# Optimization experiments

Hardware: AMD Instinct MI355X
Metric: run time of the kernel (lower is better)

Reference implementation:

```python
import jax, jax.numpy as jnp
import numpy as np

TOP_K = 2  # cfg.num_experts_per_tok
INIT_STD = 0.02


def setup_inputs() -> dict:
    key = jax.random.key(0)
    ks = jax.random.split(key, 6)
    B, S, D, F, E = 4, 2048, 1024, 4096, 8
    return {
        "residual": jax.random.normal(ks[0], (B, S, D), dtype=jnp.float32),
        "W_router": jax.random.normal(ks[1], (E, D), dtype=jnp.float32) * INIT_STD,
        "W_in": jax.random.normal(ks[2], (E, D, F), dtype=jnp.float32) * INIT_STD,
        "b_in": jnp.zeros((E, F), dtype=jnp.float32),
        "W_out": jax.random.normal(ks[3], (E, F, D), dtype=jnp.float32) * INIT_STD,
        "b_out": jnp.zeros((E, D), dtype=jnp.float32),
    }


def reference(residual, W_router, W_in, b_in, W_out, b_out):
    B, S, D = residual.shape
    E = W_router.shape[0]
    x = residual.reshape(-1, D)                      # [T, D], T = B*S

    # Router: softmax over experts, pick top-k, renormalize selected weights.
    logits = jnp.einsum('td,ed->te', x, W_router)    # [T, E]
    probs = jax.nn.softmax(logits, axis=-1)
    top_w, top_i = jax.lax.top_k(probs, TOP_K)       # [T, K]
    top_w = top_w / jnp.sum(top_w, axis=-1, keepdims=True)

    # Dense combine weights [T, E]; zero for non-selected experts.
    combine = jnp.sum(jax.nn.one_hot(top_i, E, dtype=x.dtype) * top_w[..., None], axis=1)

    # Weighted sum of expert MLP outputs (GELU experts, exact erf as in torch).
    y = jnp.zeros_like(x)
    for e in range(E):  # small fixed expert count
        h = jax.nn.gelu(x @ W_in[e] + b_in[e], approximate=False)   # [T, F]
        y = y + combine[:, e:e + 1] * (h @ W_out[e] + b_out[e])     # [T, D]
    return y.reshape(B, S, D)
```

## Files before the change

kernel.cpp:

```cpp
#include <hip/hip_runtime.h>
#include <hip/hip_bf16.h>
#include <math.h>

#define T_TOK 8192
#define DMODEL 1024
#define FFN 4096
#define NEXP 8
#define NSLOT (T_TOK * 2)
#define MAXT 136

typedef _Float16 f16;
typedef _Float16 half8 __attribute__((ext_vector_type(8)));
typedef _Float16 half4 __attribute__((ext_vector_type(4)));
typedef float f32x4 __attribute__((ext_vector_type(4)));
typedef unsigned int u32;

__device__ __forceinline__ void gll16(const void* g, void* l) {
  __builtin_amdgcn_global_load_lds(
      (const __attribute__((address_space(1))) u32*)g,
      (__attribute__((address_space(3))) u32*)l, 16, 0, 0);
}

__device__ __forceinline__ float gelu_fast(float v) {
  float x = fabsf(v) * 0.70710678118654752f;
  float t = 1.0f / (1.0f + 0.3275911f * x);
  float poly = ((((1.061405429f * t - 1.453152027f) * t + 1.421413741f) * t -
                 0.284496736f) * t + 0.254829592f) * t;
  float erf_ = 1.0f - poly * __expf(-x * x);
  erf_ = copysignf(erf_, v);
  return 0.5f * v * (1.0f + erf_);
}

__device__ __forceinline__ float gelu_exact(float v) {
  return 0.5f * v * (1.0f + erff(v * 0.70710678118654752f));
}

__device__ __forceinline__ void transq_tile(const float* __restrict__ ip,
                                            f16* __restrict__ op, int R, int C,
                                            int r0, int c0, char* smemraw) {
  float* tile = (float*)smemraw;
  int tid = threadIdx.x;
  int q = tid & 15;
  int rr = tid >> 4;
#pragma unroll
  for (int p = 0; p < 8; p++) {
    int row = rr + p * 16;
    float4 v = *(const float4*)(ip + (size_t)(r0 + row) * C + c0 + q * 4);
    int qs = (q + (row >> 3)) & 15;
    *(float4*)(tile + row * 64 + qs * 4) = v;
  }
  __syncthreads();
#pragma unroll
  for (int p = 0; p < 4; p++) {
    int idx = tid + p * 256;
    int c = idx >> 4;
    int b = idx & 15;
    half8 h;
#pragma unroll
    for (int i = 0; i < 8; i++) {
      int row = b * 8 + i;
      int qs = (((c >> 2) + b) & 15);
      h[i] = (f16)tile[row * 64 + qs * 4 + (c & 3)];
    }
    *(half8*)(op + (size_t)(c0 + c) * R + r0 + b * 8) = h;
  }
}

__global__ __launch_bounds__(256) void prepA_k(
    const float* __restrict__ x, const float* __restrict__ Wr,
    const float* __restrict__ Wi,
    int* __restrict__ sel_e, float* __restrict__ sel_w,
    f16* __restrict__ xh, f16* __restrict__ WiT) {
  __shared__ __align__(16) char smem[32768];
  if (blockIdx.x < 4096) {
    int e = blockIdx.x >> 9;
    int idx = blockIdx.x & 511;
    int rt = idx >> 6, ct = idx & 63;
    transq_tile(Wi + (size_t)e * DMODEL * FFN, WiT + (size_t)e * DMODEL * FFN,
                DMODEL, FFN, rt * 128, ct * 64, smem);
  } else {
    int rb = blockIdx.x - 4096;
    int t = rb * 4 + (threadIdx.x >> 6);
    int lane = threadIdx.x & 63;
    const float* xp = x + (size_t)t * DMODEL;
    f16* xhp = xh + (size_t)t * DMODEL;
    float p[NEXP];
#pragma unroll
    for (int e = 0; e < NEXP; e++) p[e] = 0.f;
#pragma unroll
    for (int q = 0; q < 4; q++) {
      float4 xv = *(const float4*)(xp + q * 256 + lane * 4);
      half4 h;
      h[0] = (f16)xv.x; h[1] = (f16)xv.y; h[2] = (f16)xv.z; h[3] = (f16)xv.w;
      *(half4*)(xhp + q * 256 + lane * 4) = h;
#pragma unroll
      for (int e = 0; e < NEXP; e++) {
        float4 wv = *(const float4*)(Wr + e * DMODEL + q * 256 + lane * 4);
        p[e] += xv.x * wv.x + xv.y * wv.y + xv.z * wv.z + xv.w * wv.w;
      }
    }
#pragma unroll
    for (int off = 32; off; off >>= 1) {
#pragma unroll
      for (int e = 0; e < NEXP; e++) p[e] += __shfl_xor(p[e], off);
    }
    if (lane == 0) {
      float l0 = -1e30f, l1 = -1e30f;
      int e0 = 0, e1 = 1;
#pragma unroll
      for (int e = 0; e < NEXP; e++) {
        if (p[e] > l0) { l1 = l0; e1 = e0; l0 = p[e]; e0 = e; }
        else if (p[e] > l1) { l1 = p[e]; e1 = e; }
      }
      float r = expf(l1 - l0);
      float inv = 1.f / (1.f + r);
      sel_e[t * 2] = e0;     sel_w[t * 2] = inv;
      sel_e[t * 2 + 1] = e1; sel_w[t * 2 + 1] = r * inv;
    }
  }
}

__global__ __launch_bounds__(256) void count8_k(const int* __restrict__ sel_e,
                                                int* __restrict__ counts) {
  int e = blockIdx.x;
  int tid = threadIdx.x;
  int c = 0;
  for (int i = tid; i < NSLOT; i += 256) c += (sel_e[i] == e) ? 1 : 0;
#pragma unroll
  for (int off = 32; off; off >>= 1) c += __shfl_down(c, off);
  __shared__ int red[4];
  if ((tid & 63) == 0) red[tid >> 6] = c;
  __syncthreads();
  if (tid == 0) counts[e] = red[0] + red[1] + red[2] + red[3];
}

__global__ void sched_k(int* meta) {
  int* counts = meta;
  int* fill = meta + 64;
  int* offs = meta + 128;
  int* tE = meta + 256;
  int* tR0 = meta + 512;
  int* tRows = meta + 768;
  int off = 0, nt = 0;
  for (int e = 0; e < NEXP; e++) {
    offs[e] = off;
    fill[e] = 0;
    int c = counts[e];
    for (int t0 = 0; t0 < c; t0 += 128) {
      tE[nt] = e; tR0[nt] = off + t0; tRows[nt] = min(128, c - t0); nt++;
    }
    off += c;
  }
  offs[NEXP] = off;
  for (; nt < MAXT; nt++) tE[nt] = -1;
}

__global__ __launch_bounds__(256) void scatter_k(
    const int* __restrict__ sel_e, const float* __restrict__ sel_w,
    const int* __restrict__ offs, int* fill,
    int* __restrict__ row_tok, float* __restrict__ row_w) {
  int s = blockIdx.x * 256 + threadIdx.x;
  int e = sel_e[s];
  int pos = atomicAdd(&fill[e], 1);
  int r = offs[e] + pos;
  row_tok[r] = s >> 1;
  row_w[r] = sel_w[s];
}

__global__ __launch_bounds__(256, 3) void gemm1_k(
    const f16* __restrict__ Xh, const f16* __restrict__ Wt,
    const float* __restrict__ b_in, f16* __restrict__ H,
    const int* __restrict__ meta,
    const float* __restrict__ Wo, f16* __restrict__ WoT) {
  __shared__ __align__(16) char smem[33792];

  if (blockIdx.x < 4096) {
    int e = blockIdx.x >> 9;
    int idx = blockIdx.x & 511;
    int rt = idx >> 4, ct = idx & 15;
    transq_tile(Wo + (size_t)e * DMODEL * FFN, WoT + (size_t)e * DMODEL * FFN,
                FFN, DMODEL, rt * 128, ct * 64, smem);
    return;
  }
  int bid2 = blockIdx.x - 4096;
  int xcd = bid2 & 7, bidx = bid2 >> 3;
  int wg = xcd * ((MAXT * 32) >> 3) + bidx;
  int tm = wg >> 5;
  int n0 = (wg & 31) * 128;
  int e = (meta + 256)[tm];
  if (e < 0) return;
  int row0 = (meta + 512)[tm];
  int nrows = (meta + 768)[tm];
  const int* row_tok = meta + 1024 + 2 * NSLOT;

  int tid = threadIdx.x, lane = tid & 63, wid = tid >> 6;
  int wrow = wid >> 1, wcol = wid & 1;
  int l15 = lane & 15, l4 = lane >> 4;

  u32 aoffs[4], boffs[4];
#pragma unroll
  for (int p = 0; p < 4; p++) {
    int L = tid + p * 256;
    int row = L >> 3, ch = L & 7;
    int cs = ch ^ (row & 7);
    aoffs[p] = (u32)(row_tok[min(row0 + row, NSLOT - 1)] * (DMODEL * 2) + cs * 16);
    boffs[p] = (u32)((e * FFN + n0 + row) * (DMODEL * 2) + cs * 16);
  }
  const char* gA = (const char*)Xh;
  const char* gB = (const char*)Wt;

  f32x4 acc[4][4];
#pragma unroll
  for (int m = 0; m < 4; m++)
#pragma unroll
    for (int n = 0; n < 4; n++) acc[m][n] = (f32x4)0.f;

  const int NT = DMODEL / 64;
  for (int kt = 0; kt < NT; ++kt) {
#pragma unroll
    for (int p = 0; p < 4; p++) {
      gll16(gA + aoffs[p], smem + (tid + p * 256) * 16);
      gll16(gB + boffs[p], smem + 16384 + (tid + p * 256) * 16);
      aoffs[p] += 128; boffs[p] += 128;
    }
    __syncthreads();
#pragma unroll
    for (int s = 0; s < 2; s++) {
      int swz = ((s * 4 + l4) ^ (l15 & 7)) << 4;
      const char* pA = smem + (wrow * 64 + l15) * 128 + swz;
      const char* pB = smem + 16384 + (wcol * 64 + l15) * 128 + swz;
      half8 a[4], b[4];
#pragma unroll
      for (int i = 0; i < 4; i++) a[i] = *(const half8*)(pA + i * 2048);
#pragma unroll
      for (int j = 0; j < 4; j++) b[j] = *(const half8*)(pB + j * 2048);
#pragma unroll
      for (int i = 0; i < 4; i++)
#pragma unroll
        for (int j = 0; j < 4; j++)
          acc[i][j] = __builtin_amdgcn_mfma_f32_16x16x32_f16(a[i], b[j], acc[i][j], 0, 0, 0);
    }
    __syncthreads();
  }

  float bias[4];
#pragma unroll
  for (int n = 0; n < 4; n++) bias[n] = b_in[e * FFN + n0 + wcol * 64 + n * 16 + l15];
#pragma unroll
  for (int m = 0; m < 4; m++)
#pragma unroll
    for (int n = 0; n < 4; n++)
#pragma unroll
      for (int j = 0; j < 4; j++) {
        int row = wrow * 64 + m * 16 + l4 * 4 + j;
        int col = wcol * 64 + n * 16 + l15;
        *(f16*)(smem + row * 264 + col * 2) = (f16)gelu_fast(acc[m][n][j] + bias[n]);
      }
  __syncthreads();
#pragma unroll
  for (int p = 0; p < 8; ++p) {
    int idx = tid + p * 256;
    int row = idx >> 4, cc = idx & 15;
    if (row < nrows) {
      f32x4 v = *(const f32x4*)(smem + row * 264 + cc * 16);
      __builtin_nontemporal_store(
          v, (f32x4*)(H + (size_t)(row0 + row) * FFN + n0 + cc * 8));
    }
  }
}

__global__ __launch_bounds__(256, 3) void gemm2_k(
    const f16* __restrict__ H, const f16* __restrict__ Wt,
    const float* __restrict__ b_out, float* __restrict__ out,
    const int* __restrict__ meta) {
  int xcd = blockIdx.x & 7, bidx = blockIdx.x >> 3;
  int wg = xcd * (gridDim.x >> 3) + bidx;
  int tm = wg >> 4;
  int r4 = wg & 15;
  int n0 = (r4 & 7) * 128;
  int ks = r4 >> 3;
  int e = (meta + 256)[tm];
  if (e < 0) return;
  int row0 = (meta + 512)[tm];
  int nrows = (meta + 768)[tm];
  const int* row_tok = meta + 1024 + 2 * NSLOT;
  const float* row_w = (const float*)(meta + 1024 + 3 * NSLOT);

  __shared__ __align__(16) char smem[32768];

  int tid = threadIdx.x, lane = tid & 63, wid = tid >> 6;
  int wrow = wid >> 1, wcol = wid & 1;
  int l15 = lane & 15, l4 = lane >> 4;
  u32 k0b = (u32)(ks * (FFN / 2) * 2);

  u32 aoffs[4], boffs[4];
#pragma unroll
  for (int p = 0; p < 4; p++) {
    int L = tid + p * 256;
    int row = L >> 3, ch = L & 7;
    int cs = ch ^ (row & 7);
    aoffs[p] = (u32)((u32)min(row0 + row, NSLOT - 1) * (FFN * 2) + k0b + cs * 16);
    boffs[p] = (u32)((u32)(e * DMODEL + n0 + row) * (FFN * 2) + k0b + cs * 16);
  }
  const char* gA = (const char*)H;
  const char* gB = (const char*)Wt;

  f32x4 acc[4][4];
#pragma unroll
  for (int m = 0; m < 4; m++)
#pragma unroll
    for (int n = 0; n < 4; n++) acc[m][n] = (f32x4)0.f;

  const int NT = (FFN / 2) / 64;
  for (int kt = 0; kt < NT; ++kt) {
#pragma unroll
    for (int p = 0; p < 4; p++) {
      gll16(gA + aoffs[p], smem + (tid + p * 256) * 16);
      gll16(gB + boffs[p], smem + 16384 + (tid + p * 256) * 16);
      aoffs[p] += 128; boffs[p] += 128;
    }
    __syncthreads();
#pragma unroll
    for (int s = 0; s < 2; s++) {
      int swz = ((s * 4 + l4) ^ (l15 & 7)) << 4;
      const char* pA = smem + (wrow * 64 + l15) * 128 + swz;
      const char* pB = smem + 16384 + (wcol * 64 + l15) * 128 + swz;
      half8 a[4], b[4];
#pragma unroll
      for (int i = 0; i < 4; i++) a[i] = *(const half8*)(pA + i * 2048);
#pragma unroll
      for (int j = 0; j < 4; j++) b[j] = *(const half8*)(pB + j * 2048);
#pragma unroll
      for (int i = 0; i < 4; i++)
#pragma unroll
        for (int j = 0; j < 4; j++)
          acc[i][j] = __builtin_amdgcn_mfma_f32_16x16x32_f16(a[i], b[j], acc[i][j], 0, 0, 0);
    }
    __syncthreads();
  }

  float bias[4];
#pragma unroll
  for (int n = 0; n < 4; n++)
    bias[n] = (ks == 0) ? b_out[e * DMODEL + n0 + wcol * 64 + n * 16 + l15] : 0.f;
#pragma unroll
  for (int m = 0; m < 4; m++)
#pragma unroll
    for (int j = 0; j < 4; j++) {
      int r = wrow * 64 + m * 16 + l4 * 4 + j;
      if (r < nrows) {
        int rg = row0 + r;
        int tok = row_tok[rg];
        float w = row_w[rg];
#pragma unroll
        for (int n = 0; n < 4; n++)
          atomicAdd(out + (size_t)tok * DMODEL + n0 + wcol * 64 + n * 16 + l15,
                    w * (acc[m][n][j] + bias[n]));
      }
    }
}

__global__ __launch_bounds__(256) void naive_k(
    const float* __restrict__ x, const float* __restrict__ W_in,
    const float* __restrict__ b_in, const float* __restrict__ W_out,
    const float* __restrict__ b_out, const int* __restrict__ sel_e,
    const float* __restrict__ sel_w, float* __restrict__ out) {
  int s = blockIdx.x;
  int t = s >> 1;
  int e = sel_e[s];
  float w = sel_w[s];
  __shared__ float xs[DMODEL];
  __shared__ float hs[FFN];
  int tid = threadIdx.x;
  for (int d = tid; d < DMODEL; d += 256) xs[d] = x[(size_t)t * DMODEL + d];
  __syncthreads();
  for (int f = tid; f < FFN; f += 256) {
    float a = b_in[e * FFN + f];
    const float* wp = W_in + (size_t)e * DMODEL * FFN + f;
    for (int d = 0; d < DMODEL; d++) a += xs[d] * wp[(size_t)d * FFN];
    hs[f] = gelu_exact(a);
  }
  __syncthreads();
  for (int d = tid; d < DMODEL; d += 256) {
    float a = b_out[e * DMODEL + d];
    const float* wp = W_out + (size_t)e * FFN * DMODEL + d;
    for (int f = 0; f < FFN; f++) a += hs[f] * wp[(size_t)f * DMODEL];
    atomicAdd(&out[(size_t)t * DMODEL + d], w * a);
  }
}

__global__ __launch_bounds__(256) void router_k(
    const float* __restrict__ x, const float* __restrict__ Wr,
    int* __restrict__ sel_e, float* __restrict__ sel_w) {
  int t = blockIdx.x * 4 + (threadIdx.x >> 6);
  int lane = threadIdx.x & 63;
  const float* xp = x + (size_t)t * DMODEL;
  float p[NEXP];
#pragma unroll
  for (int e = 0; e < NEXP; e++) p[e] = 0.f;
#pragma unroll
  for (int i = 0; i < DMODEL / 64; i++) {
    float xv = xp[lane + i * 64];
#pragma unroll
    for (int e = 0; e < NEXP; e++) p[e] += xv * Wr[e * DMODEL + lane + i * 64];
  }
#pragma unroll
  for (int off = 32; off; off >>= 1) {
#pragma unroll
    for (int e = 0; e < NEXP; e++) p[e] += __shfl_xor(p[e], off);
  }
  if (lane == 0) {
    float l0 = -1e30f, l1 = -1e30f;
    int e0 = 0, e1 = 1;
#pragma unroll
    for (int e = 0; e < NEXP; e++) {
      if (p[e] > l0) { l1 = l0; e1 = e0; l0 = p[e]; e0 = e; }
      else if (p[e] > l1) { l1 = p[e]; e1 = e; }
    }
    float r = expf(l1 - l0);
    float inv = 1.f / (1.f + r);
    sel_e[t * 2] = e0;     sel_w[t * 2] = inv;
    sel_e[t * 2 + 1] = e1; sel_w[t * 2 + 1] = r * inv;
  }
}

extern "C" void kernel_launch(void* const* d_in, const int* in_sizes, int n_in,
                              void* d_out, int out_size, void* d_ws, size_t ws_size,
                              hipStream_t stream) {
  const float* residual = (const float*)d_in[0];
  const float* W_router = (const float*)d_in[1];
  const float* W_in = (const float*)d_in[2];
  const float* b_in = (const float*)d_in[3];
  const float* W_out = (const float*)d_in[4];
  const float* b_out = (const float*)d_in[5];
  float* out = (float*)d_out;

  char* ws = (char*)d_ws;
  int* meta = (int*)ws;
  size_t off = (size_t)1 << 20;
  f16* Xh = (f16*)(ws + off); off += (size_t)T_TOK * DMODEL * 2;
  f16* Wih = (f16*)(ws + off); off += (size_t)NEXP * DMODEL * FFN * 2;
  f16* Woh = (f16*)(ws + off); off += (size_t)NEXP * DMODEL * FFN * 2;
  f16* H = (f16*)(ws + off); off += (size_t)NSLOT * FFN * 2;
  off += 65536;
  bool fast = ws_size >= off;

  int* sel_e = meta + 1024;
  float* sel_w = (float*)(meta + 1024 + NSLOT);
  int* row_tok = meta + 1024 + 2 * NSLOT;
  float* row_w = (float*)(meta + 1024 + 3 * NSLOT);

  hipMemsetAsync(meta, 0, 4096, stream);
  hipMemsetAsync(d_out, 0, (size_t)out_size * sizeof(float), stream);

  if (fast) {
    prepA_k<<<4096 + T_TOK / 4, 256, 0, stream>>>(
        residual, W_router, W_in, sel_e, sel_w, Xh, Wih);
    count8_k<<<NEXP, 256, 0, stream>>>(sel_e, meta);
    sched_k<<<1, 1, 0, stream>>>(meta);
    scatter_k<<<NSLOT / 256, 256, 0, stream>>>(sel_e, sel_w, meta + 128, meta + 64,
                                               row_tok, row_w);
    gemm1_k<<<4096 + MAXT * 32, 256, 0, stream>>>(Xh, Wih, b_in, H, meta,
                                                  W_out, Woh);
    gemm2_k<<<MAXT * 16, 256, 0, stream>>>(H, Woh, b_out, out, meta);
  } else {
    router_k<<<T_TOK / 4, 256, 0, stream>>>(residual, W_router, sel_e, sel_w);
    naive_k<<<NSLOT, 256, 0, stream>>>(residual, W_in, b_in, W_out, b_out,
                                       sel_e, sel_w, out);
  }
}
```

Measured before the change: 565.4 us.

## Fuse expert count and schedule kernels, reorder gemm1 blocks, raise occupancy

Replaces the per-expert count kernel and the single-thread schedule kernel with one kernel. It counts all eight experts in one pass and then builds the tile schedule, which removes a launch and a serial dependency. In gemm1 the GEMM blocks now come before the W_out transpose blocks, so the compute work dispatches first and the transpose fills in afterwards. Launch bounds for both GEMMs go from 3 to 4 waves per SIMD, which may force fewer registers and cause spills.

```diff
diff --git a/kernel.cpp b/kernel.cpp
--- a/kernel.cpp
+++ b/kernel.cpp
@@ -120,39 +120,53 @@
   }
 }
 
-__global__ __launch_bounds__(256) void count8_k(const int* __restrict__ sel_e,
-                                                int* __restrict__ counts) {
-  int e = blockIdx.x;
+__global__ __launch_bounds__(256) void count_sched_k(
+    const int* __restrict__ sel_e, int* __restrict__ meta) {
+  __shared__ int cnts[NEXP];
   int tid = threadIdx.x;
-  int c = 0;
-  for (int i = tid; i < NSLOT; i += 256) c += (sel_e[i] == e) ? 1 : 0;
-#pragma unroll
-  for (int off = 32; off; off >>= 1) c += __shfl_down(c, off);
-  __shared__ int red[4];
-  if ((tid & 63) == 0) red[tid >> 6] = c;
-  __syncthreads();
-  if (tid == 0) counts[e] = red[0] + red[1] + red[2] + red[3];
-}
-
-__global__ void sched_k(int* meta) {
-  int* counts = meta;
-  int* fill = meta + 64;
-  int* offs = meta + 128;
-  int* tE = meta + 256;
-  int* tR0 = meta + 512;
-  int* tRows = meta + 768;
-  int off = 0, nt = 0;
-  for (int e = 0; e < NEXP; e++) {
-    offs[e] = off;
-    fill[e] = 0;
-    int c = counts[e];
-    for (int t0 = 0; t0 < c; t0 += 128) {
-      tE[nt] = e; tR0[nt] = off + t0; tRows[nt] = min(128, c - t0); nt++;
-    }
-    off += c;
-  }
-  offs[NEXP] = off;
-  for (; nt < MAXT; nt++) tE[nt] = -1;
+  if (tid < NEXP) cnts[tid] = 0;
+  __syncthreads();
+  int c0 = 0, c1 = 0, c2 = 0, c3 = 0, c4 = 0, c5 = 0, c6 = 0, c7 = 0;
+  for (int i = tid; i < NSLOT; i += 256) {
+    int v = sel_e[i];
+    c0 += (v == 0); c1 += (v == 1); c2 += (v == 2); c3 += (v == 3);
+    c4 += (v == 4); c5 += (v == 5); c6 += (v == 6); c7 += (v == 7);
+  }
+#pragma unroll
+  for (int off = 32; off; off >>= 1) {
+    c0 += __shfl_down(c0, off); c1 += __shfl_down(c1, off);
+    c2 += __shfl_down(c2, off); c3 += __shfl_down(c3, off);
+    c4 += __shfl_down(c4, off); c5 += __shfl_down(c5, off);
+    c6 += __shfl_down(c6, off); c7 += __shfl_down(c7, off);
+  }
+  if ((tid & 63) == 0) {
+    atomicAdd(&cnts[0], c0); atomicAdd(&cnts[1], c1);
+    atomicAdd(&cnts[2], c2); atomicAdd(&cnts[3], c3);
+    atomicAdd(&cnts[4], c4); atomicAdd(&cnts[5], c5);
+    atomicAdd(&cnts[6], c6); atomicAdd(&cnts[7], c7);
+  }
+  __syncthreads();
+  if (tid == 0) {
+    int* counts = meta;
+    int* fill = meta + 64;
+    int* offs = meta + 128;
+    int* tE = meta + 256;
+    int* tR0 = meta + 512;
+    int* tRows = meta + 768;
+    int off = 0, nt = 0;
+    for (int e = 0; e < NEXP; e++) {
+      counts[e] = cnts[e];
+      offs[e] = off;
+      fill[e] = 0;
+      int c = cnts[e];
+      for (int t0 = 0; t0 < c; t0 += 128) {
+        tE[nt] = e; tR0[nt] = off + t0; tRows[nt] = min(128, c - t0); nt++;
+      }
+      off += c;
+    }
+    offs[NEXP] = off;
+    for (; nt < MAXT; nt++) tE[nt] = -1;
+  }
 }
 
 __global__ __launch_bounds__(256) void scatter_k(
@@ -167,22 +181,23 @@
   row_w[r] = sel_w[s];
 }
 
-__global__ __launch_bounds__(256, 3) void gemm1_k(
+__global__ __launch_bounds__(256, 4) void gemm1_k(
     const f16* __restrict__ Xh, const f16* __restrict__ Wt,
     const float* __restrict__ b_in, f16* __restrict__ H,
     const int* __restrict__ meta,
     const float* __restrict__ Wo, f16* __restrict__ WoT) {
   __shared__ __align__(16) char smem[33792];
 
-  if (blockIdx.x < 4096) {
-    int e = blockIdx.x >> 9;
-    int idx = blockIdx.x & 511;
+  if (blockIdx.x >= MAXT * 32) {
+    int bid = blockIdx.x - MAXT * 32;
+    int e = bid >> 9;
+    int idx = bid & 511;
     int rt = idx >> 4, ct = idx & 15;
     transq_tile(Wo + (size_t)e * DMODEL * FFN, WoT + (size_t)e * DMODEL * FFN,
                 FFN, DMODEL, rt * 128, ct * 64, smem);
     return;
   }
-  int bid2 = blockIdx.x - 4096;
+  int bid2 = blockIdx.x;
   int xcd = bid2 & 7, bidx = bid2 >> 3;
   int wg = xcd * ((MAXT * 32) >> 3) + bidx;
   int tm = wg >> 5;
@@ -269,7 +284,7 @@
   }
 }
 
-__global__ __launch_bounds__(256, 3) void gemm2_k(
+__global__ __launch_bounds__(256, 4) void gemm2_k(
     const f16* __restrict__ H, const f16* __restrict__ Wt,
     const float* __restrict__ b_out, float* __restrict__ out,
     const int* __restrict__ meta) {
@@ -456,11 +471,10 @@
   if (fast) {
     prepA_k<<<4096 + T_TOK / 4, 256, 0, stream>>>(
         residual, W_router, W_in, sel_e, sel_w, Xh, Wih);
-    count8_k<<<NEXP, 256, 0, stream>>>(sel_e, meta);
-    sched_k<<<1, 1, 0, stream>>>(meta);
+    count_sched_k<<<1, 256, 0, stream>>>(sel_e, meta);
     scatter_k<<<NSLOT / 256, 256, 0, stream>>>(sel_e, sel_w, meta + 128, meta + 64,
                                                row_tok, row_w);
-    gemm1_k<<<4096 + MAXT * 32, 256, 0, stream>>>(Xh, Wih, b_in, H, meta,
+    gemm1_k<<<MAXT * 32 + 4096, 256, 0, stream>>>(Xh, Wih, b_in, H, meta,
                                                   W_out, Woh);
     gemm2_k<<<MAXT * 16, 256, 0, stream>>>(H, Woh, b_out, out, meta);
   } else {
```

After: 560.7 us. No clear change (-0.8%).
